# Kernel optimization log

Hardware: AMD Instinct MI355X
Metric: run time of the kernel (lower is better)

Reference implementation:

```python
import jax, jax.numpy as jnp
import numpy as np


def setup_inputs() -> dict:
    key = jax.random.key(0)
    ks = jax.random.split(key, 8)
    B, C, H, W = 4, 128, 128, 128
    C8 = C // 8
    x = jax.random.normal(ks[0], (B, C, H, W), jnp.float32)
    # 1x1 conv weights as [out, in] matrices + biases
    Wq = jax.random.normal(ks[1], (C8, C), jnp.float32) * 0.05
    bq = jax.random.normal(ks[2], (C8,), jnp.float32) * 0.01
    Wk = jax.random.normal(ks[3], (C8, C), jnp.float32) * 0.05
    bk = jax.random.normal(ks[4], (C8,), jnp.float32) * 0.01
    Wv = jax.random.normal(ks[5], (C, C), jnp.float32) * 0.05
    bv = jax.random.normal(ks[6], (C,), jnp.float32) * 0.01
    # nn.Parameter(torch.zeros(1)) in the original; use nonzero so output/grads are nontrivial
    gamma = jax.random.normal(ks[7], (), jnp.float32) * 0.1
    return {"x": x, "Wq": Wq, "bq": bq, "Wk": Wk, "bk": bk,
            "Wv": Wv, "bv": bv, "gamma": gamma}


def reference(x, Wq, bq, Wk, bk, Wv, bv, gamma):
    # x: [b, c, h, w]
    b, c, h, w = x.shape
    # 1x1 convs == channel contractions
    q = jnp.einsum('bchw,oc->bohw', x, Wq) + bq[None, :, None, None]  # [b,c8,h,w]
    k = jnp.einsum('bchw,oc->bohw', x, Wk) + bk[None, :, None, None]  # [b,c8,h,w]
    v = jnp.einsum('bchw,oc->bohw', x, Wv) + bv[None, :, None, None]  # [b,c, h,w]

    # column (height) attention logits: e_h[b, h1, w, h2], diagonal masked to -inf
    e_h = jnp.einsum('bcxw,bcyw->bxwy', q, k)
    diag = jnp.eye(h, dtype=bool)  # [h1, h2]
    e_h = jnp.where(diag[:, None, :], -jnp.inf, e_h)
    # row (width) attention logits: e_w[b, h, w1, w2]
    e_w = jnp.einsum('bchx,bchy->bhxy', q, k)

    # joint softmax over concatenated (h2 + w2) axis
    attn = jax.nn.softmax(jnp.concatenate([e_h, e_w], axis=3), axis=3)  # [b,h,w,h+w]
    attn_h = attn[..., :h]   # [b, h1, w, h2]
    attn_w = attn[..., h:]   # [b, h, w1, w2]

    # aggregate values along columns and rows
    out_h = jnp.einsum('bcyw,bxwy->bcxw', v, attn_h)  # [b,c,h,w]
    out_w = jnp.einsum('bchy,bhxy->bchx', v, attn_w)  # [b,c,h,w]

    out = gamma * (out_h + out_w) + x
    # return_attn: stack([b h2 h1 w, b w2 h w1], dim=1)
    return_attn = jnp.stack([jnp.transpose(attn_h, (0, 3, 1, 2)),
                             jnp.transpose(attn_w, (0, 3, 1, 2))], axis=1)
    return out, return_attn
```

## Files before the change

kernel.cpp:

```cpp
#include <hip/hip_runtime.h>
#include <math.h>

#define HW_ 16384
#define SLOT_ 2097152ULL
#define BSTR_ 4194304ULL

typedef __attribute__((ext_vector_type(8))) short short8v;
typedef __attribute__((ext_vector_type(4))) float f32x4;

__device__ __forceinline__ unsigned short f2bf(float f) {
  unsigned int u = __float_as_uint(f);
  u = (u + 0x7FFFu + ((u >> 16) & 1u)) >> 16;
  return (unsigned short)u;
}
__device__ __forceinline__ float bf2f(unsigned short h) {
  return __uint_as_float(((unsigned int)h) << 16);
}

__global__ void qkv_proj(const float* __restrict__ x,
                         const float* __restrict__ Wq, const float* __restrict__ bq,
                         const float* __restrict__ Wk, const float* __restrict__ bk,
                         const float* __restrict__ Wv, const float* __restrict__ bv,
                         float* __restrict__ qT, float* __restrict__ kT,
                         unsigned short* __restrict__ vA0,
                         unsigned short* __restrict__ Ew, float* __restrict__ rsw) {
  __shared__ float WT[128][36];
  __shared__ float BUF[8448];
  float (*Wc)[132] = (float(*)[132])BUF;
  float (*Xc)[132] = (float(*)[132])(BUF + 4224);
  int t = threadIdx.x;
  for (int i = t; i < 4096; i += 256) {
    int o = i >> 7, c = i & 127;
    WT[c][o] = (o < 16) ? Wq[o * 128 + c] : Wk[(o - 16) * 128 + c];
  }
  int blk = blockIdx.x;
  int b = blk >> 7, h = blk & 127;
  int p0 = h * 128;
  int tc = t & 15, tx = t >> 4;
  float acc[8][8];
#pragma unroll
  for (int ci = 0; ci < 8; ++ci) {
    float bvv = bv[tc * 8 + ci];
#pragma unroll
    for (int pi = 0; pi < 8; ++pi) acc[ci][pi] = bvv;
  }
  float accqk[2][8];
#pragma unroll
  for (int e = 0; e < 2; ++e) {
    int och = tc * 2 + e;
    float bias = (och < 16) ? bq[och] : bk[och - 16];
#pragma unroll
    for (int pi = 0; pi < 8; ++pi) accqk[e][pi] = bias;
  }
  int c2 = t >> 1, part = t & 1;
  __syncthreads();
  for (int k0 = 0; k0 < 128; k0 += 32) {
#pragma unroll
    for (int qq = 0; qq < 4; ++qq) {
      int y4 = part * 16 + qq * 4;
      float4 w4 = *(const float4*)&Wv[c2 * 128 + k0 + y4];
      Wc[y4 + 0][c2] = w4.x;
      Wc[y4 + 1][c2] = w4.y;
      Wc[y4 + 2][c2] = w4.z;
      Wc[y4 + 3][c2] = w4.w;
    }
#pragma unroll
    for (int r = 0; r < 4; ++r) {
      int idx = r * 1024 + t * 4;
      int kl = idx >> 7, ccc = idx & 127;
      *(float4*)&Xc[kl][ccc] =
          *(const float4*)&x[(size_t)b * 128 * HW_ + (size_t)(k0 + kl) * HW_ + p0 + ccc];
    }
    __syncthreads();
    for (int kl = 0; kl < 32; ++kl) {
      float wa[8], xa[8];
      *(float4*)(wa)     = *(const float4*)&Wc[kl][tc * 8];
      *(float4*)(wa + 4) = *(const float4*)&Wc[kl][tc * 8 + 4];
      *(float4*)(xa)     = *(const float4*)&Xc[kl][tx * 8];
      *(float4*)(xa + 4) = *(const float4*)&Xc[kl][tx * 8 + 4];
      float wq0 = WT[k0 + kl][tc * 2];
      float wq1 = WT[k0 + kl][tc * 2 + 1];
#pragma unroll
      for (int ci = 0; ci < 8; ++ci)
#pragma unroll
        for (int pi = 0; pi < 8; ++pi)
          acc[ci][pi] = fmaf(wa[ci], xa[pi], acc[ci][pi]);
#pragma unroll
      for (int pi = 0; pi < 8; ++pi) {
        accqk[0][pi] = fmaf(wq0, xa[pi], accqk[0][pi]);
        accqk[1][pi] = fmaf(wq1, xa[pi], accqk[1][pi]);
      }
    }
    __syncthreads();
  }
#pragma unroll
  for (int ci = 0; ci < 8; ++ci) {
    union { unsigned short us[8]; uint4 v; } pk;
#pragma unroll
    for (int pi = 0; pi < 8; ++pi) pk.us[pi] = f2bf(acc[ci][pi]);
    *(uint4*)&vA0[(size_t)(b * 128 + h) * 16384 + (size_t)(tc * 8 + ci) * 128 + tx * 8] = pk.v;
  }
  float (*QKs)[36] = (float(*)[36])BUF;
#pragma unroll
  for (int e = 0; e < 2; ++e)
#pragma unroll
    for (int pi = 0; pi < 8; ++pi)
      QKs[tx * 8 + pi][tc * 2 + e] = accqk[e][pi];
  __syncthreads();
  {
    int px = t >> 1, sel = t & 1;
    const float* qr = &QKs[px][sel * 16];
    float4 r0 = *(const float4*)(qr);
    float4 r1 = *(const float4*)(qr + 4);
    float4 r2 = *(const float4*)(qr + 8);
    float4 r3 = *(const float4*)(qr + 12);
    float* dstT = (sel ? kT : qT) + ((size_t)(b * HW_ + px * 128 + h)) * 16;
    *(float4*)(dstT)      = r0;
    *(float4*)(dstT + 4)  = r1;
    *(float4*)(dstT + 8)  = r2;
    *(float4*)(dstT + 12) = r3;
  }
  float (*Qs)[132] = (float(*)[132])&WT[0][0];
  float (*Ks)[132] = (float(*)[132])(&WT[0][0] + 2112);
  {
    int cc = t & 15, pb = (t >> 4) * 8;
#pragma unroll
    for (int u = 0; u < 8; ++u) {
      Qs[cc][pb + u] = QKs[pb + u][cc];
      Ks[cc][pb + u] = QKs[pb + u][16 + cc];
    }
  }
  __syncthreads();
  {
    int tr = (t >> 4) * 8;
    int ty = (t & 15) * 8;
    float sc_[8][8] = {{0.f}};
#pragma unroll
    for (int c = 0; c < 16; ++c) {
      float qa[8], ka[8];
      *(float4*)(qa)     = *(const float4*)&Qs[c][tr];
      *(float4*)(qa + 4) = *(const float4*)&Qs[c][tr + 4];
      *(float4*)(ka)     = *(const float4*)&Ks[c][ty];
      *(float4*)(ka + 4) = *(const float4*)&Ks[c][ty + 4];
#pragma unroll
      for (int u = 0; u < 8; ++u)
#pragma unroll
        for (int v = 0; v < 8; ++v)
          sc_[u][v] = fmaf(qa[u], ka[v], sc_[u][v]);
    }
    float rp[8];
#pragma unroll
    for (int u = 0; u < 8; ++u) {
      rp[u] = 0.f;
#pragma unroll
      for (int v = 0; v < 8; ++v) {
        float e = __expf(sc_[u][v]);
        sc_[u][v] = e;
        rp[u] += e;
      }
    }
    unsigned short* out = Ew + (size_t)blk * 16384;
#pragma unroll
    for (int u = 0; u < 8; ++u) {
      union { unsigned short us[8]; uint4 v; } pk;
#pragma unroll
      for (int v = 0; v < 8; ++v) pk.us[v] = f2bf(sc_[u][v]);
      *(uint4*)&out[(tr + u) * 128 + ty] = pk.v;
    }
#pragma unroll
    for (int u = 0; u < 8; ++u) {
      rp[u] += __shfl_xor(rp[u], 1);
      rp[u] += __shfl_xor(rp[u], 2);
      rp[u] += __shfl_xor(rp[u], 4);
      rp[u] += __shfl_xor(rp[u], 8);
    }
    if ((t & 15) == 0) {
#pragma unroll
      for (int u = 0; u < 8; ++u) rsw[(size_t)blk * 128 + tr + u] = rp[u];
    }
  }
}

__global__ void score_h(const float* __restrict__ Q, const float* __restrict__ K,
                        unsigned short* __restrict__ E, float* __restrict__ rsum,
                        size_t ebs, size_t eoff) {
  __shared__ float Qs[16][132];
  __shared__ float Ks[16][132];
  int slab = blockIdx.x;
  int b = slab >> 7, s = slab & 127;
  const float* qb = Q + (size_t)slab * 2048;
  const float* kb = K + (size_t)slab * 2048;
  int t = threadIdx.x;
  int cc = t & 15;
  int pb = (t >> 4) * 8;
#pragma unroll
  for (int u = 0; u < 8; ++u) {
    Qs[cc][pb + u] = qb[(size_t)(pb + u) * 16 + cc];
    Ks[cc][pb + u] = kb[(size_t)(pb + u) * 16 + cc];
  }
  __syncthreads();
  int tr = (t >> 4) * 8;
  int ty = (t & 15) * 8;
  float acc[8][8] = {{0.f}};
#pragma unroll
  for (int c = 0; c < 16; ++c) {
    float qa[8], ka[8];
    *(float4*)(qa)     = *(const float4*)&Qs[c][tr];
    *(float4*)(qa + 4) = *(const float4*)&Qs[c][tr + 4];
    *(float4*)(ka)     = *(const float4*)&Ks[c][ty];
    *(float4*)(ka + 4) = *(const float4*)&Ks[c][ty + 4];
#pragma unroll
    for (int u = 0; u < 8; ++u)
#pragma unroll
      for (int v = 0; v < 8; ++v)
        acc[u][v] = fmaf(qa[u], ka[v], acc[u][v]);
  }
  float rp[8];
#pragma unroll
  for (int u = 0; u < 8; ++u) {
    rp[u] = 0.f;
#pragma unroll
    for (int v = 0; v < 8; ++v) {
      float e = __expf(acc[u][v]);
      if ((tr + u) == (ty + v)) e = 0.f;
      acc[u][v] = e;
      rp[u] += e;
    }
  }
  unsigned short* out = E + (size_t)b * ebs + eoff + (size_t)s * 16384;
#pragma unroll
  for (int u = 0; u < 8; ++u) {
    union { unsigned short us[8]; uint4 v; } pk;
#pragma unroll
    for (int v = 0; v < 8; ++v) pk.us[v] = f2bf(acc[u][v]);
    *(uint4*)&out[(tr + u) * 128 + ty] = pk.v;
  }
#pragma unroll
  for (int u = 0; u < 8; ++u) {
    rp[u] += __shfl_xor(rp[u], 1);
    rp[u] += __shfl_xor(rp[u], 2);
    rp[u] += __shfl_xor(rp[u], 4);
    rp[u] += __shfl_xor(rp[u], 8);
  }
  if ((t & 15) == 0) {
#pragma unroll
    for (int u = 0; u < 8; ++u) rsum[(size_t)slab * 128 + tr + u] = rp[u];
  }
}

__global__ void trans_v(const unsigned short* __restrict__ vA0, unsigned short* __restrict__ vA1,
                        const float* __restrict__ rsw, const float* __restrict__ rsh,
                        float* __restrict__ dij, float* __restrict__ dji) {
  __shared__ unsigned short tile[64][65];
  int blk = blockIdx.x;
  int q = blk & 3, c = (blk >> 2) & 127, b = blk >> 9;
  int h0 = (q >> 1) * 64, w0 = (q & 1) * 64;
  int t = threadIdx.x, lane = t & 63, r0 = (t >> 6) * 16;
  for (int r = r0; r < r0 + 16; ++r)
    tile[r][lane] = vA0[(size_t)(b * 128 + h0 + r) * 16384 + c * 128 + w0 + lane];
  __syncthreads();
  for (int r = r0; r < r0 + 16; ++r)
    vA1[(size_t)(b * 128 + w0 + r) * 16384 + c * 128 + h0 + lane] = tile[lane][r];
  if (blk < 256) {
    int p = blk * 256 + t;
    int bb = p >> 14, rem = p & 16383, i = rem >> 7, j = rem & 127;
    float d = rsw[p] + rsh[(size_t)bb * HW_ + j * 128 + i];
    float r = 1.0f / d;
    dij[p] = r;
    dji[(size_t)bb * HW_ + j * 128 + i] = r;
  }
}

__global__ void pv2(const unsigned short* __restrict__ vA0,
                    const unsigned short* __restrict__ vA1,
                    const unsigned short* __restrict__ Ew,
                    const unsigned short* __restrict__ EhB,
                    const float* __restrict__ dij, const float* __restrict__ dji,
                    unsigned short* __restrict__ ow, unsigned short* __restrict__ ohb) {
  __shared__ unsigned short Al[128][44];
  __shared__ unsigned short Bl[128][44];
  int blk = blockIdx.x;
  int m = blk >> 9;
  int slab = blk & 511;
  int s = slab & 127, b = slab >> 7;
  int t = threadIdx.x;
  int wv = t >> 6, l = t & 63;
  int wc = (wv >> 1) * 64, wx = (wv & 1) * 64;
  const unsigned short* vs = (m ? vA1 : vA0) + (size_t)slab * 16384;
  const unsigned short* es = m ? (EhB + (size_t)b * 8388608 + 4194304 + (size_t)s * 16384)
                               : (Ew + (size_t)slab * 16384);
  const float* invd = m ? dji : dij;
  f32x4 acc[4][4];
#pragma unroll
  for (int mi = 0; mi < 4; ++mi)
#pragma unroll
    for (int ni = 0; ni < 4; ++ni) acc[mi][ni] = (f32x4){0.f, 0.f, 0.f, 0.f};
  int lrow = t >> 2, lq = t & 3;
  int lm = l & 15, lk = (l >> 4) * 4;
  for (int y0 = 0; y0 < 128; y0 += 32) {
#pragma unroll
    for (int r = 0; r < 2; ++r) {
      int rr = lrow + r * 64;
      uint4 av = *(const uint4*)(vs + (size_t)rr * 128 + y0 + lq * 8);
      uint4 bv = *(const uint4*)(es + (size_t)rr * 128 + y0 + lq * 8);
      *(uint2*)&Al[rr][lq * 8]     = make_uint2(av.x, av.y);
      *(uint2*)&Al[rr][lq * 8 + 4] = make_uint2(av.z, av.w);
      *(uint2*)&Bl[rr][lq * 8]     = make_uint2(bv.x, bv.y);
      *(uint2*)&Bl[rr][lq * 8 + 4] = make_uint2(bv.z, bv.w);
    }
    __syncthreads();
    short8v af[4], bf[4];
#pragma unroll
    for (int mi = 0; mi < 4; ++mi) {
      const unsigned short* ap = &Al[wc + mi * 16 + lm][lk];
      union { uint2 p[2]; short8v v; } u;
      u.p[0] = *(const uint2*)ap;
      u.p[1] = *(const uint2*)(ap + 16);
      af[mi] = u.v;
    }
#pragma unroll
    for (int ni = 0; ni < 4; ++ni) {
      const unsigned short* bp = &Bl[wx + ni * 16 + lm][lk];
      union { uint2 p[2]; short8v v; } u;
      u.p[0] = *(const uint2*)bp;
      u.p[1] = *(const uint2*)(bp + 16);
      bf[ni] = u.v;
    }
#pragma unroll
    for (int mi = 0; mi < 4; ++mi)
#pragma unroll
      for (int ni = 0; ni < 4; ++ni)
        acc[mi][ni] = __builtin_amdgcn_mfma_f32_16x16x32_bf16(af[mi], bf[ni], acc[mi][ni], 0, 0, 0);
    __syncthreads();
  }
  int lr4 = (l >> 4) * 4;
  unsigned short* dst = m ? ohb : ow;
#pragma unroll
  for (int ni = 0; ni < 4; ++ni) {
    int xx = wx + ni * 16 + lm;
    float idv = invd[(size_t)(b * 128 + s) * 128 + xx];
#pragma unroll
    for (int mi = 0; mi < 4; ++mi) {
#pragma unroll
      for (int r = 0; r < 4; ++r) {
        int c = wc + mi * 16 + lr4 + r;
        size_t idx = m ? ((size_t)b * 8388608 + (size_t)s * 16384 + (size_t)c * 128 + xx)
                       : ((((size_t)(b * 128 + c)) * 128 + s) * 128 + xx);
        dst[idx] = f2bf(acc[mi][ni][r] * idv);
      }
    }
  }
}

__global__ void merge2(const unsigned short* __restrict__ ow,
                       const unsigned short* __restrict__ ohp,
                       const float* __restrict__ xin, const float* __restrict__ gamma,
                       float* __restrict__ outp) {
  __shared__ float tile[64][65];
  int blk = blockIdx.x;
  int q = blk & 3, c = (blk >> 2) & 127, b = blk >> 9;
  int h0 = (q >> 1) * 64, w0 = (q & 1) * 64;
  int t = threadIdx.x, lane = t & 63, r0 = (t >> 6) * 16;
  for (int r = r0; r < r0 + 16; ++r)
    tile[r][lane] =
        bf2f(ohp[(size_t)b * 8388608ULL + (size_t)(w0 + r) * 16384 + c * 128 + h0 + lane]);
  __syncthreads();
  float g = gamma[0];
  for (int r = r0; r < r0 + 16; ++r) {
    size_t a = (((size_t)(b * 128 + c)) * 128 + h0 + r) * 128 + w0 + lane;
    outp[a] = g * (bf2f(ow[a]) + tile[lane][r]) + xin[a];
  }
}

template <int HM>
__global__ void ret_write(const unsigned short* __restrict__ src, const float* __restrict__ invd,
                          float* __restrict__ retb, size_t sbs, size_t soff) {
  __shared__ float tile[128][129];
  __shared__ float idv[128];
  int slab = blockIdx.x;
  int b = slab >> 7, i = slab & 127;
  int t = threadIdx.x;
  const unsigned short* sp = src + (size_t)b * sbs + soff;
#pragma unroll
  for (int r = 0; r < 8; ++r) {
    int idx = r * 2048 + t * 8;
    int j = idx >> 7, y = idx & 127;
    uint4 raw;
    if (HM == 0)
      raw = *(const uint4*)(sp + (size_t)i * 16384 + j * 128 + y);
    else
      raw = *(const uint4*)(sp + (size_t)j * 16384 + i * 128 + y);
    unsigned int wd[4] = {raw.x, raw.y, raw.z, raw.w};
#pragma unroll
    for (int e = 0; e < 4; ++e) {
      tile[j][y + 2 * e]     = __uint_as_float((wd[e] & 0xFFFFu) << 16);
      tile[j][y + 2 * e + 1] = __uint_as_float(wd[e] & 0xFFFF0000u);
    }
  }
  if (t < 128) idv[t] = invd[(size_t)slab * 128 + t];
  __syncthreads();
  float* dp = retb + (size_t)b * BSTR_ + (HM == 0 ? SLOT_ : 0);
#pragma unroll
  for (int r = 0; r < 16; ++r) {
    int idx = r * 1024 + t * 4;
    int y = idx >> 7, j = idx & 127;
    float4 o;
    o.x = tile[j][y]     * idv[j];
    o.y = tile[j + 1][y] * idv[j + 1];
    o.z = tile[j + 2][y] * idv[j + 2];
    o.w = tile[j + 3][y] * idv[j + 3];
    *(float4*)&dp[(size_t)y * 16384 + i * 128 + j] = o;
  }
}

extern "C" void kernel_launch(void* const* d_in, const int* in_sizes, int n_in,
                              void* d_out, int out_size, void* d_ws, size_t ws_size,
                              hipStream_t stream) {
  const float* x     = (const float*)d_in[0];
  const float* Wq    = (const float*)d_in[1];
  const float* bq    = (const float*)d_in[2];
  const float* Wk    = (const float*)d_in[3];
  const float* bk    = (const float*)d_in[4];
  const float* Wv    = (const float*)d_in[5];
  const float* bv    = (const float*)d_in[6];
  const float* gamma = (const float*)d_in[7];

  float* outp = (float*)d_out;
  float* retb = outp + (size_t)8388608;
  unsigned short* ohb = (unsigned short*)retb;
  unsigned short* ehb = (unsigned short*)retb;

  float* ws      = (float*)d_ws;
  float* qT      = ws + (size_t)2097152;
  float* kT      = ws + (size_t)3145728;
  unsigned short* ow  = (unsigned short*)ws;
  unsigned short* vA0 = (unsigned short*)(ws + (size_t)4194304);
  unsigned short* vA1 = (unsigned short*)(ws + (size_t)8388608);
  unsigned short* E_w = (unsigned short*)(ws + (size_t)12582912);
  float* rsum_w  = ws + (size_t)16777216;
  float* rsum_h  = ws + (size_t)16842752;
  float* invd_ij = ws + (size_t)16908288;
  float* invd_ji = ws + (size_t)16973824;

  qkv_proj<<<512, 256, 0, stream>>>(x, Wq, bq, Wk, bk, Wv, bv,
                                    qT, kT, vA0, E_w, rsum_w);
  score_h<<<512, 256, 0, stream>>>(qT, kT, ehb, rsum_h,
                                   (size_t)8388608, (size_t)4194304);
  trans_v<<<2048, 256, 0, stream>>>(vA0, vA1, rsum_w, rsum_h, invd_ij, invd_ji);
  pv2<<<1024, 256, 0, stream>>>(vA0, vA1, E_w, ehb, invd_ij, invd_ji, ow, ohb);
  merge2<<<2048, 256, 0, stream>>>(ow, ohb, x, gamma, outp);
  ret_write<1><<<512, 256, 0, stream>>>(ehb, invd_ij, retb, (size_t)8388608, (size_t)4194304);
  ret_write<0><<<512, 256, 0, stream>>>(E_w, invd_ij, retb, (size_t)2097152, (size_t)0);
}
```

Before: 134.5 us.

## Split fused QKV projection into separate QK-score and V projection kernels

```diff
diff --git a/kernel.cpp b/kernel.cpp
--- a/kernel.cpp
+++ b/kernel.cpp
@@ -17,17 +17,14 @@
   return __uint_as_float(((unsigned int)h) << 16);
 }
 
-__global__ void qkv_proj(const float* __restrict__ x,
+__global__ void qk_score(const float* __restrict__ x,
                          const float* __restrict__ Wq, const float* __restrict__ bq,
                          const float* __restrict__ Wk, const float* __restrict__ bk,
-                         const float* __restrict__ Wv, const float* __restrict__ bv,
                          float* __restrict__ qT, float* __restrict__ kT,
-                         unsigned short* __restrict__ vA0,
                          unsigned short* __restrict__ Ew, float* __restrict__ rsw) {
   __shared__ float WT[128][36];
-  __shared__ float BUF[8448];
-  float (*Wc)[132] = (float(*)[132])BUF;
-  float (*Xc)[132] = (float(*)[132])(BUF + 4224);
+  __shared__ float BUF[4608];
+  float (*Xc)[132] = (float(*)[132])BUF;
   int t = threadIdx.x;
   for (int i = t; i < 4096; i += 256) {
     int o = i >> 7, c = i & 127;
@@ -37,13 +34,6 @@
   int b = blk >> 7, h = blk & 127;
   int p0 = h * 128;
   int tc = t & 15, tx = t >> 4;
-  float acc[8][8];
-#pragma unroll
-  for (int ci = 0; ci < 8; ++ci) {
-    float bvv = bv[tc * 8 + ci];
-#pragma unroll
-    for (int pi = 0; pi < 8; ++pi) acc[ci][pi] = bvv;
-  }
   float accqk[2][8];
 #pragma unroll
   for (int e = 0; e < 2; ++e) {
@@ -52,18 +42,8 @@
 #pragma unroll
     for (int pi = 0; pi < 8; ++pi) accqk[e][pi] = bias;
   }
-  int c2 = t >> 1, part = t & 1;
   __syncthreads();
   for (int k0 = 0; k0 < 128; k0 += 32) {
-#pragma unroll
-    for (int qq = 0; qq < 4; ++qq) {
-      int y4 = part * 16 + qq * 4;
-      float4 w4 = *(const float4*)&Wv[c2 * 128 + k0 + y4];
-      Wc[y4 + 0][c2] = w4.x;
-      Wc[y4 + 1][c2] = w4.y;
-      Wc[y4 + 2][c2] = w4.z;
-      Wc[y4 + 3][c2] = w4.w;
-    }
 #pragma unroll
     for (int r = 0; r < 4; ++r) {
       int idx = r * 1024 + t * 4;
@@ -73,32 +53,18 @@
     }
     __syncthreads();
     for (int kl = 0; kl < 32; ++kl) {
-      float wa[8], xa[8];
-      *(float4*)(wa)     = *(const float4*)&Wc[kl][tc * 8];
-      *(float4*)(wa + 4) = *(const float4*)&Wc[kl][tc * 8 + 4];
+      float xa[8];
       *(float4*)(xa)     = *(const float4*)&Xc[kl][tx * 8];
       *(float4*)(xa + 4) = *(const float4*)&Xc[kl][tx * 8 + 4];
       float wq0 = WT[k0 + kl][tc * 2];
       float wq1 = WT[k0 + kl][tc * 2 + 1];
 #pragma unroll
-      for (int ci = 0; ci < 8; ++ci)
-#pragma unroll
-        for (int pi = 0; pi < 8; ++pi)
-          acc[ci][pi] = fmaf(wa[ci], xa[pi], acc[ci][pi]);
-#pragma unroll
       for (int pi = 0; pi < 8; ++pi) {
         accqk[0][pi] = fmaf(wq0, xa[pi], accqk[0][pi]);
         accqk[1][pi] = fmaf(wq1, xa[pi], accqk[1][pi]);
       }
     }
     __syncthreads();
-  }
-#pragma unroll
-  for (int ci = 0; ci < 8; ++ci) {
-    union { unsigned short us[8]; uint4 v; } pk;
-#pragma unroll
-    for (int pi = 0; pi < 8; ++pi) pk.us[pi] = f2bf(acc[ci][pi]);
-    *(uint4*)&vA0[(size_t)(b * 128 + h) * 16384 + (size_t)(tc * 8 + ci) * 128 + tx * 8] = pk.v;
   }
   float (*QKs)[36] = (float(*)[36])BUF;
 #pragma unroll
@@ -178,6 +144,67 @@
 #pragma unroll
       for (int u = 0; u < 8; ++u) rsw[(size_t)blk * 128 + tr + u] = rp[u];
     }
+  }
+}
+
+__global__ void v_bf(const float* __restrict__ x, const float* __restrict__ Wv,
+                     const float* __restrict__ bv, unsigned short* __restrict__ vA0) {
+  __shared__ float Wc[32][68];
+  __shared__ float Xc[32][132];
+  int blk = blockIdx.x;
+  int half = blk & 1;
+  int h = (blk >> 1) & 127;
+  int b = blk >> 8;
+  int p0 = h * 128;
+  int cbase = half * 64;
+  int t = threadIdx.x;
+  int tc = t & 15, tx = t >> 4;
+  float acc[4][8];
+#pragma unroll
+  for (int ci = 0; ci < 4; ++ci) {
+    float bvv = bv[cbase + tc * 4 + ci];
+#pragma unroll
+    for (int pi = 0; pi < 8; ++pi) acc[ci][pi] = bvv;
+  }
+  int c2 = t >> 2, part = t & 3;
+  for (int k0 = 0; k0 < 128; k0 += 32) {
+#pragma unroll
+    for (int qq = 0; qq < 2; ++qq) {
+      int y4 = part * 4 + qq * 16;
+      float4 w4 = *(const float4*)&Wv[(cbase + c2) * 128 + k0 + y4];
+      Wc[y4 + 0][c2] = w4.x;
+      Wc[y4 + 1][c2] = w4.y;
+      Wc[y4 + 2][c2] = w4.z;
+      Wc[y4 + 3][c2] = w4.w;
+    }
+#pragma unroll
+    for (int r = 0; r < 4; ++r) {
+      int idx = r * 1024 + t * 4;
+      int kl = idx >> 7, ccc = idx & 127;
+      *(float4*)&Xc[kl][ccc] =
+          *(const float4*)&x[(size_t)b * 128 * HW_ + (size_t)(k0 + kl) * HW_ + p0 + ccc];
+    }
+    __syncthreads();
+    for (int kl = 0; kl < 32; ++kl) {
+      float wa[4], xa[8];
+      *(float4*)(wa)     = *(const float4*)&Wc[kl][tc * 4];
+      *(float4*)(xa)     = *(const float4*)&Xc[kl][tx * 8];
+      *(float4*)(xa + 4) = *(const float4*)&Xc[kl][tx * 8 + 4];
+#pragma unroll
+      for (int ci = 0; ci < 4; ++ci)
+#pragma unroll
+        for (int pi = 0; pi < 8; ++pi)
+          acc[ci][pi] = fmaf(wa[ci], xa[pi], acc[ci][pi]);
+    }
+    __syncthreads();
+  }
+#pragma unroll
+  for (int ci = 0; ci < 4; ++ci) {
+    union { unsigned short us[8]; uint4 v; } pk;
+#pragma unroll
+    for (int pi = 0; pi < 8; ++pi) pk.us[pi] = f2bf(acc[ci][pi]);
+    *(uint4*)&vA0[(size_t)(b * 128 + h) * 16384 + (size_t)(cbase + tc * 4 + ci) * 128 + tx * 8] =
+        pk.v;
   }
 }
 
@@ -442,8 +469,8 @@
   float* invd_ij = ws + (size_t)16908288;
   float* invd_ji = ws + (size_t)16973824;
 
-  qkv_proj<<<512, 256, 0, stream>>>(x, Wq, bq, Wk, bk, Wv, bv,
-                                    qT, kT, vA0, E_w, rsum_w);
+  qk_score<<<512, 256, 0, stream>>>(x, Wq, bq, Wk, bk, qT, kT, E_w, rsum_w);
+  v_bf<<<1024, 256, 0, stream>>>(x, Wv, bv, vA0);
   score_h<<<512, 256, 0, stream>>>(qT, kT, ehb, rsum_h,
                                    (size_t)8388608, (size_t)4194304);
   trans_v<<<2048, 256, 0, stream>>>(vA0, vA1, rsum_w, rsum_h, invd_ij, invd_ji);
```

Result: slower. 170.4 us (+26.6%).
